# Kernel tuning notes

Measured on AMD Instinct MI355X. Metric: run time of the kernel, lower is better.

Reference implementation:

```python
import jax, jax.numpy as jnp
import numpy as np

D_MODEL, D_STATE, D_CONV, EXPAND = 1024, 16, 4, 2
D_INNER = EXPAND * D_MODEL
DT_RANK = max(16, D_MODEL // 16)
B_SZ, T_LEN = 2, 2048


def setup_inputs() -> dict:
    key = jax.random.key(0)
    ks = jax.random.split(key, 12)
    s = lambda fan: 1.0 / np.sqrt(fan)
    x = jax.random.normal(ks[0], (B_SZ, T_LEN, D_MODEL), jnp.float32)
    sigma2 = jax.random.uniform(ks[1], (B_SZ, T_LEN, 1), jnp.float32)
    W_in = jax.random.normal(ks[2], (D_MODEL, 2 * D_INNER), jnp.float32) * s(D_MODEL)
    conv_w = jax.random.normal(ks[3], (D_CONV, 1, D_INNER), jnp.float32) * s(D_CONV)
    conv_b = jax.random.normal(ks[4], (D_INNER,), jnp.float32) * 0.01
    W_xproj = jax.random.normal(ks[5], (D_INNER, 2 * D_STATE + DT_RANK), jnp.float32) * s(D_INNER)
    W_delta = jax.random.normal(ks[6], (D_MODEL, D_INNER), jnp.float32) * s(D_MODEL)
    b_delta = jax.random.normal(ks[7], (D_INNER,), jnp.float32) * 0.01
    A_log = jnp.log(jnp.tile(jnp.arange(1, D_STATE + 1, dtype=jnp.float32), (D_INNER, 1)))
    D_param = jnp.ones((D_INNER,), jnp.float32)
    W_out = jax.random.normal(ks[8], (D_INNER, D_MODEL), jnp.float32) * s(D_INNER)
    alpha = jnp.float32(1.0)
    return {"x": x, "sigma2": sigma2, "W_in": W_in, "conv_w": conv_w, "conv_b": conv_b,
            "W_xproj": W_xproj, "W_delta": W_delta, "b_delta": b_delta, "A_log": A_log,
            "D_param": D_param, "W_out": W_out, "alpha": alpha}


def _forward(x, sigma2, W_in, conv_w, conv_b, W_xproj, W_delta, b_delta, A_log, D_param, W_out, alpha):
    # in_proj and split
    xz = jnp.einsum('btd,de->bte', x, W_in)
    u, z = jnp.split(xz, 2, axis=-1)                      # (B,T,d_inner) each
    # causal depthwise conv1d (left pad d_conv-1, truncate to T)
    u = jax.lax.conv_general_dilated(
        u, conv_w, window_strides=(1,), padding=[(D_CONV - 1, 0)],
        dimension_numbers=('NHC', 'HIO', 'NHC'), feature_group_count=D_INNER) + conv_b
    u = jax.nn.silu(u)
    # x_proj -> B, C (delta_raw_proj branch is unused in custom-delta path)
    x_dbl = jnp.einsum('bti,ij->btj', u, W_xproj)
    Bp = x_dbl[..., :D_STATE]                              # (B,T,d_state)
    Cp = x_dbl[..., D_STATE:2 * D_STATE]                   # (B,T,d_state)
    # quality-gated custom delta
    delta_raw = jax.nn.softplus(jnp.einsum('btd,di->bti', x, W_delta) + b_delta)
    delta = delta_raw * jnp.exp(-alpha * sigma2)           # (B,T,d_inner)
    A = -jnp.exp(A_log)                                    # (d_inner,d_state)
    # discretize
    dA = jnp.exp(delta[..., None] * A)                     # (B,T,d_inner,d_state)
    dBu = delta[..., None] * Bp[:, :, None, :] * u[..., None]

    def step(h, inp):
        dA_t, dBu_t, c_t = inp                             # (B,di,ds),(B,di,ds),(B,ds)
        h = dA_t * h + dBu_t
        y_t = jnp.sum(h * c_t[:, None, :], axis=-1)        # (B,d_inner)
        return h, y_t

    h0 = jnp.zeros((x.shape[0], D_INNER, D_STATE), dtype=u.dtype)
    _, ys = jax.lax.scan(step, h0, (jnp.moveaxis(dA, 1, 0), jnp.moveaxis(dBu, 1, 0), jnp.moveaxis(Cp, 1, 0)))
    y = jnp.moveaxis(ys, 0, 1) + u * D_param               # (B,T,d_inner)
    y = y * jax.nn.silu(z)
    return jnp.einsum('bti,id->btd', y, W_out)


def reference(x, sigma2, W_in, conv_w, conv_b, W_xproj, W_delta, b_delta, A_log, D_param, W_out, alpha):
    return _forward(x, sigma2, W_in, conv_w, conv_b, W_xproj, W_delta, b_delta, A_log, D_param, W_out, alpha)
```

## Files before the change

### kernel.cpp

```cpp
#include <hip/hip_runtime.h>
#include <math.h>


constexpr int D_MODEL = 1024;
constexpr int D_STATE = 16;
constexpr int D_CONV  = 4;
constexpr int D_INNER = 2048;
constexpr int XPROJ_W = 96;
constexpr int B_SZ = 2, T_LEN = 2048;
constexpr int ROWS = B_SZ * T_LEN;
constexpr int NCHUNK = 64, CHUNK = T_LEN / NCHUNK;

typedef unsigned short ushort_t;
typedef __bf16 bf16x8 __attribute__((ext_vector_type(8)));
typedef float f32x4 __attribute__((ext_vector_type(4)));

__device__ __forceinline__ ushort_t f2bf(float f) {
  unsigned int u = __float_as_uint(f);
  u = (u + 0x7fffu + ((u >> 16) & 1u)) >> 16;
  return (ushort_t)u;
}
__device__ __forceinline__ float bf2f(ushort_t h) {
  return __uint_as_float(((unsigned int)h) << 16);
}

__device__ __forceinline__ void gload16(const void* g, void* l) {
  __builtin_amdgcn_global_load_lds(
      (const __attribute__((address_space(1))) void*)g,
      (__attribute__((address_space(3))) void*)l, 16, 0, 0);
}

__global__ __launch_bounds__(256)
void convert_all_kernel(const float* __restrict__ x,
                        const float* __restrict__ W_in,
                        const float* __restrict__ W_delta,
                        const float* __restrict__ W_out,
                        ushort_t* __restrict__ xb, ushort_t* __restrict__ WiT,
                        ushort_t* __restrict__ WdT, ushort_t* __restrict__ WoT)
{
  __shared__ float tile[32][33];
  const int blk = blockIdx.x;
  const int tid = threadIdx.x;
  if (blk < 4096) {
    const int i = blk * 256 + tid;
    const float4 v = ((const float4*)x)[i];
    ushort_t tmp[4] = {f2bf(v.x), f2bf(v.y), f2bf(v.z), f2bf(v.w)};
    ((uint2*)xb)[i] = *(const uint2*)tmp;
    return;
  }
  const float* in;
  ushort_t* out;
  int R, C, t;
  if (blk < 8192)      { in = W_in;    out = WiT; R = 1024; C = 4096; t = blk - 4096;  }
  else if (blk < 10240){ in = W_delta; out = WdT; R = 1024; C = 2048; t = blk - 8192;  }
  else                 { in = W_out;   out = WoT; R = 2048; C = 1024; t = blk - 10240; }
  const int tpr = C / 32;
  const int c0 = (t % tpr) * 32, r0 = (t / tpr) * 32;
  const int tx = tid & 31, ty = tid >> 5;
#pragma unroll
  for (int i = 0; i < 32; i += 8)
    tile[ty + i][tx] = in[(size_t)(r0 + ty + i) * C + c0 + tx];
  __syncthreads();
#pragma unroll
  for (int i = 0; i < 32; i += 8)
    out[(size_t)(c0 + ty + i) * R + r0 + tx] = f2bf(tile[tx][ty + i]);
}

template <int MODE, int BM>
__global__ __launch_bounds__(256)
void gemm_t(const ushort_t* __restrict__ A, const ushort_t* __restrict__ Bt,
            const int lda, const int ldb, const int KT,
            ushort_t* __restrict__ outB, float* __restrict__ outF,
            const float* __restrict__ bias, const float* __restrict__ sigma2,
            const float* __restrict__ alphap)
{
  constexpr int MREP = (BM == 32) ? 2 : 4;
  constexpr int NREP = (BM == 128) ? 4 : 2;
  constexpr int RT = BM + 128;
  constexpr int CH = RT / 32;

  __shared__ __align__(16) ushort_t As[BM * 64];
  __shared__ __align__(16) ushort_t Bs[128 * 64];
  const int tid = threadIdx.x;
  const int wave = tid >> 6, lane = tid & 63;
  const int lc = lane & 15, lr = lane >> 4;
  const int m0 = blockIdx.y * BM, n0 = blockIdx.x * 128;
  const int N = gridDim.x * 128;
  const int arow = (BM == 128) ? ((wave >> 1) * 64) : 0;
  const int bcol = (BM == 128) ? ((wave & 1) * 64) : (wave * 32);

  f32x4 acc[MREP][NREP];
#pragma unroll
  for (int i = 0; i < MREP; ++i)
#pragma unroll
    for (int j = 0; j < NREP; ++j) acc[i][j] = (f32x4)0.f;

  const int rlane = lane >> 3;
  const int clane = (lane & 7) * 8;

  for (int kt = 0; kt < KT; ++kt) {
    if (kt) __syncthreads();
    const int k0 = kt * 64;
#pragma unroll
    for (int i = 0; i < CH; ++i) {
      const int r0c = (wave * CH + i) * 8;
      if (r0c < BM) {
        gload16(A + (size_t)(m0 + r0c + rlane) * lda + k0 + clane,
                &As[r0c * 64]);
      } else {
        const int br = r0c - BM;
        gload16(Bt + (size_t)(n0 + br + rlane) * ldb + k0 + clane,
                &Bs[br * 64]);
      }
    }
    __syncthreads();
#pragma unroll
    for (int ks = 0; ks < 2; ++ks) {
      bf16x8 af[MREP], bfr[NREP];
#pragma unroll
      for (int mi = 0; mi < MREP; ++mi)
        af[mi] = *(const bf16x8*)
            &As[(arow + mi * 16 + lc) * 64 + ks * 32 + lr * 8];
#pragma unroll
      for (int ni = 0; ni < NREP; ++ni)
        bfr[ni] = *(const bf16x8*)
            &Bs[(bcol + ni * 16 + lc) * 64 + ks * 32 + lr * 8];
#pragma unroll
      for (int mi = 0; mi < MREP; ++mi)
#pragma unroll
        for (int ni = 0; ni < NREP; ++ni)
          acc[mi][ni] = __builtin_amdgcn_mfma_f32_16x16x32_bf16(
              af[mi], bfr[ni], acc[mi][ni], 0, 0, 0);
    }
  }

  const float alphaV = (MODE == 2) ? alphap[0] : 0.f;
#pragma unroll
  for (int mi = 0; mi < MREP; ++mi) {
    const int rowb = m0 + arow + mi * 16 + lr * 4;
#pragma unroll
    for (int ni = 0; ni < NREP; ++ni) {
      const int col = n0 + bcol + ni * 16 + lc;
      f32x4 v = acc[mi][ni];
      if (MODE == 0) {
#pragma unroll
        for (int r = 0; r < 4; ++r)
          outB[(size_t)(rowb + r) * N + col] = f2bf(v[r]);
      } else if (MODE == 2) {
        const float bv = bias[col];
#pragma unroll
        for (int r = 0; r < 4; ++r) {
          const float xv = v[r] + bv;
          const float sp = (xv > 20.f) ? xv : log1pf(__expf(xv));
          outB[(size_t)(rowb + r) * N + col] =
              f2bf(sp * __expf(-alphaV * sigma2[rowb + r]));
        }
      } else {
#pragma unroll
        for (int r = 0; r < 4; ++r)
          outF[(size_t)(rowb + r) * N + col] = v[r];
      }
    }
  }
}

__device__ __forceinline__ void decay_powers(float d, float (&dA)[16])
{
  const float q1 = __expf(-d);
  const float q2 = q1 * q1, q3 = q2 * q1, q4 = q2 * q2;
  const float q8 = q4 * q4, q12 = q8 * q4;
  dA[0] = q1;        dA[1] = q2;        dA[2] = q3;        dA[3] = q4;
  dA[4] = q4 * q1;   dA[5] = q4 * q2;   dA[6] = q4 * q3;   dA[7] = q8;
  dA[8] = q8 * q1;   dA[9] = q8 * q2;   dA[10] = q8 * q3;  dA[11] = q12;
  dA[12] = q12 * q1; dA[13] = q12 * q2; dA[14] = q12 * q3; dA[15] = q12 * q4;
}

__global__ __launch_bounds__(256)
void conv_xproj_kernel(const ushort_t* __restrict__ xzb,
                       const float* __restrict__ cw,
                       const float* __restrict__ cb,
                       const float* __restrict__ Wx,
                       ushort_t* __restrict__ u, float* __restrict__ BC)
{
  __shared__ float us[8][D_INNER];
  __shared__ float red[8][8][32];
  const int tid = threadIdx.x;
  const int b = blockIdx.y;
  const int t0 = blockIdx.x * 8;
  const int ch0 = tid * 8;

  float wtk[4][8], bs[8];
#pragma unroll
  for (int k = 0; k < 4; ++k) {
    float4 wa = *(const float4*)&cw[k * D_INNER + ch0];
    float4 wb = *(const float4*)&cw[k * D_INNER + ch0 + 4];
    wtk[k][0] = wa.x; wtk[k][1] = wa.y; wtk[k][2] = wa.z; wtk[k][3] = wa.w;
    wtk[k][4] = wb.x; wtk[k][5] = wb.y; wtk[k][6] = wb.z; wtk[k][7] = wb.w;
  }
  {
    float4 ba = *(const float4*)&cb[ch0];
    float4 bb = *(const float4*)&cb[ch0 + 4];
    bs[0] = ba.x; bs[1] = ba.y; bs[2] = ba.z; bs[3] = ba.w;
    bs[4] = bb.x; bs[5] = bb.y; bs[6] = bb.z; bs[7] = bb.w;
  }

#pragma unroll
  for (int r = 0; r < 8; ++r) {
    const int t = t0 + r;
    float acc[8];
#pragma unroll
    for (int j = 0; j < 8; ++j) acc[j] = bs[j];
#pragma unroll
    for (int k = 0; k < 4; ++k) {
      const int tt = t + k - 3;
      if (tt >= 0) {
        uint4 raw = *(const uint4*)
            &xzb[(size_t)(b * T_LEN + tt) * (2 * D_INNER) + ch0];
        const ushort_t* hp = (const ushort_t*)&raw;
#pragma unroll
        for (int j = 0; j < 8; ++j)
          acc[j] = fmaf(bf2f(hp[j]), wtk[k][j], acc[j]);
      }
    }
    ushort_t ub[8];
#pragma unroll
    for (int j = 0; j < 8; ++j) {
      const float ss = acc[j] / (1.f + __expf(-acc[j]));
      us[r][ch0 + j] = ss;
      ub[j] = f2bf(ss);
    }
    *(uint4*)&u[(size_t)(b * T_LEN + t) * D_INNER + ch0] = *(const uint4*)ub;
  }
  __syncthreads();

  const int j = tid & 31, chunk = tid >> 5;
  float p[8] = {0.f, 0.f, 0.f, 0.f, 0.f, 0.f, 0.f, 0.f};
  const float* WxC = Wx + j;
  for (int i = 0; i < 256; ++i) {
    const int k = chunk * 256 + i;
    const float w = WxC[(size_t)k * XPROJ_W];
#pragma unroll
    for (int r = 0; r < 8; ++r) p[r] = fmaf(us[r][k], w, p[r]);
  }
#pragma unroll
  for (int r = 0; r < 8; ++r) red[r][chunk][j] = p[r];
  __syncthreads();
  {
    const int r = tid >> 5, jj = tid & 31;
    float ssum = 0.f;
#pragma unroll
    for (int c = 0; c < 8; ++c) ssum += red[r][c][jj];
    BC[(size_t)(b * T_LEN + t0 + r) * 32 + jj] = ssum;
  }
}

__global__ __launch_bounds__(256)
void scan1_kernel(const ushort_t* __restrict__ delta,
                  const ushort_t* __restrict__ u,
                  const float* __restrict__ BC,
                  float* __restrict__ hEnd, float* __restrict__ sumD)
{
  const int c = blockIdx.x * 256 + threadIdx.x;
  const int b = blockIdx.y;
  const int j = blockIdx.z;
  float h[D_STATE];
#pragma unroll
  for (int n = 0; n < D_STATE; ++n) h[n] = 0.f;
  float sd = 0.f;
  const int t0 = j * CHUNK;
  for (int t = t0; t < t0 + CHUNK; ++t) {
    const int row = b * T_LEN + t;
    const float d = bf2f(delta[(size_t)row * D_INNER + c]);
    const float uu = bf2f(u[(size_t)row * D_INNER + c]);
    sd += d;
    const float du = d * uu;
    float dA[16];
    decay_powers(d, dA);
    const float4* bp4 = (const float4*)&BC[(size_t)row * 32];
    float4 b0 = bp4[0], b1 = bp4[1], b2 = bp4[2], b3 = bp4[3];
    const float bp[16] = {b0.x, b0.y, b0.z, b0.w, b1.x, b1.y, b1.z, b1.w,
                          b2.x, b2.y, b2.z, b2.w, b3.x, b3.y, b3.z, b3.w};
#pragma unroll
    for (int n = 0; n < D_STATE; ++n)
      h[n] = fmaf(dA[n], h[n], du * bp[n]);
  }
  const size_t base = ((size_t)b * D_INNER + c) * NCHUNK + j;
#pragma unroll
  for (int n = 0; n < D_STATE; ++n) hEnd[base * 16 + n] = h[n];
  sumD[base] = sd;
}

__global__ __launch_bounds__(256)
void scan2_kernel(float* __restrict__ hEnd, const float* __restrict__ sumD)
{
  const int idx = blockIdx.x * 256 + threadIdx.x;
  const int n = idx & 15;
  const int c = (idx >> 4) & (D_INNER - 1);
  const int b = idx >> 15;
  const float an = -(float)(n + 1);
  float H = 0.f;
  for (int j = 0; j < NCHUNK; ++j) {
    const size_t base = ((size_t)b * D_INNER + c) * NCHUNK + j;
    const float he = hEnd[base * 16 + n];
    const float sd = sumD[base];
    hEnd[base * 16 + n] = H;
    H = fmaf(__expf(an * sd), H, he);
  }
}

__global__ __launch_bounds__(256)
void scan3_kernel(const ushort_t* __restrict__ delta,
                  const ushort_t* __restrict__ u,
                  const float* __restrict__ BC,
                  const float* __restrict__ hStart,
                  const ushort_t* __restrict__ xzb,
                  const float* __restrict__ Dp, ushort_t* __restrict__ yb)
{
  const int c = blockIdx.x * 256 + threadIdx.x;
  const int b = blockIdx.y;
  const int j = blockIdx.z;
  float h[D_STATE];
  const size_t base = ((size_t)b * D_INNER + c) * NCHUNK + j;
#pragma unroll
  for (int n = 0; n < D_STATE; ++n) h[n] = hStart[base * 16 + n];
  const float dpc = Dp[c];
  const int t0 = j * CHUNK;
  for (int t = t0; t < t0 + CHUNK; ++t) {
    const int row = b * T_LEN + t;
    const float d = bf2f(delta[(size_t)row * D_INNER + c]);
    const float uu = bf2f(u[(size_t)row * D_INNER + c]);
    const float du = d * uu;
    float dA[16];
    decay_powers(d, dA);
    const float4* bc4 = (const float4*)&BC[(size_t)row * 32];
    float4 b0 = bc4[0], b1 = bc4[1], b2 = bc4[2], b3 = bc4[3];
    float4 c0 = bc4[4], c1 = bc4[5], c2 = bc4[6], c3 = bc4[7];
    const float bp[16] = {b0.x, b0.y, b0.z, b0.w, b1.x, b1.y, b1.z, b1.w,
                          b2.x, b2.y, b2.z, b2.w, b3.x, b3.y, b3.z, b3.w};
    const float cp[16] = {c0.x, c0.y, c0.z, c0.w, c1.x, c1.y, c1.z, c1.w,
                          c2.x, c2.y, c2.z, c2.w, c3.x, c3.y, c3.z, c3.w};
    float y = 0.f;
#pragma unroll
    for (int n = 0; n < D_STATE; ++n) {
      h[n] = fmaf(dA[n], h[n], du * bp[n]);
      y = fmaf(h[n], cp[n], y);
    }
    y = fmaf(uu, dpc, y);
    const float z = bf2f(xzb[(size_t)row * (2 * D_INNER) + D_INNER + c]);
    y *= z / (1.f + __expf(-z));
    yb[(size_t)row * D_INNER + c] = f2bf(y);
  }
}

extern "C" void kernel_launch(void* const* d_in, const int* in_sizes, int n_in,
                              void* d_out, int out_size, void* d_ws,
                              size_t ws_size, hipStream_t stream)
{
  const float* x       = (const float*)d_in[0];
  const float* sigma2  = (const float*)d_in[1];
  const float* W_in    = (const float*)d_in[2];
  const float* conv_w  = (const float*)d_in[3];
  const float* conv_b  = (const float*)d_in[4];
  const float* W_xproj = (const float*)d_in[5];
  const float* W_delta = (const float*)d_in[6];
  const float* b_delta = (const float*)d_in[7];
  const float* D_param = (const float*)d_in[9];
  const float* W_out   = (const float*)d_in[10];
  const float* alpha   = (const float*)d_in[11];
  float* out = (float*)d_out;

  char* ws = (char*)d_ws;
  ushort_t* xzb  = (ushort_t*)(ws);
  ushort_t* u    = (ushort_t*)(ws + ((size_t)32  << 20));
  ushort_t* dyb  = (ushort_t*)(ws + ((size_t)48  << 20));
  float*    BC   = (float*)   (ws + ((size_t)64  << 20));
  float*    hEnd = (float*)   (ws + ((size_t)65  << 20));
  float*    sumD = (float*)   (ws + ((size_t)81  << 20));
  ushort_t* xb   = (ushort_t*)(ws + ((size_t)82  << 20));
  ushort_t* WiT  = (ushort_t*)(ws + ((size_t)90  << 20));
  ushort_t* WdT  = (ushort_t*)(ws + ((size_t)98  << 20));
  ushort_t* WoT  = (ushort_t*)(ws + ((size_t)102 << 20));
  ushort_t* yb   = (ushort_t*)(ws + ((size_t)106 << 20));

  convert_all_kernel<<<12288, 256, 0, stream>>>(x, W_in, W_delta, W_out, xb,
                                                WiT, WdT, WoT);
  gemm_t<0, 128><<<dim3(4096 / 128, ROWS / 128), 256, 0, stream>>>(
      xb, WiT, 1024, 1024, 16, xzb, nullptr, nullptr, nullptr, nullptr);
  gemm_t<2, 64><<<dim3(2048 / 128, ROWS / 64), 256, 0, stream>>>(
      xb, WdT, 1024, 1024, 16, dyb, nullptr, b_delta, sigma2, alpha);
  conv_xproj_kernel<<<dim3(T_LEN / 8, B_SZ), 256, 0, stream>>>(
      xzb, conv_w, conv_b, W_xproj, u, BC);
  scan1_kernel<<<dim3(D_INNER / 256, B_SZ, NCHUNK), 256, 0, stream>>>(
      dyb, u, BC, hEnd, sumD);
  scan2_kernel<<<(B_SZ * D_INNER * D_STATE) / 256, 256, 0, stream>>>(hEnd,
                                                                     sumD);
  scan3_kernel<<<dim3(D_INNER / 256, B_SZ, NCHUNK), 256, 0, stream>>>(
      dyb, u, BC, hEnd, xzb, D_param, yb);
  gemm_t<1, 32><<<dim3(1024 / 128, ROWS / 32), 256, 0, stream>>>(
      yb, WoT, 2048, 2048, 32, nullptr, out, nullptr, nullptr, nullptr);
}
```

Before: 243.8 us.

## Pipeline GEMM loads with triple buffering and fuse independent stages into combined launches

The GEMM core now uses a three-stage LDS ring with K-step 32, manual vmcnt waits and raw barriers, so global loads overlap MFMA work. Independent work is packed into shared launches: the W_delta and W_out transposes run beside the in_proj GEMM, and the conv+xproj runs beside the delta GEMM. Other changes: the scan chunk count is halved, the conv tile is stored as bf16 in LDS, and the out-projection uses 64-row tiles. The goal is fewer launches, less idle time and better latency hiding. The cost is heterogeneous blocks within a launch, possible load imbalance, and less parallelism in the scan.

```diff
diff --git a/kernel.cpp b/kernel.cpp
--- a/kernel.cpp
+++ b/kernel.cpp
@@ -9,7 +9,7 @@
 constexpr int XPROJ_W = 96;
 constexpr int B_SZ = 2, T_LEN = 2048;
 constexpr int ROWS = B_SZ * T_LEN;
-constexpr int NCHUNK = 64, CHUNK = T_LEN / NCHUNK;
+constexpr int NCHUNK = 32, CHUNK = T_LEN / NCHUNK;
 
 typedef unsigned short ushort_t;
 typedef __bf16 bf16x8 __attribute__((ext_vector_type(8)));
@@ -30,64 +30,32 @@
       (__attribute__((address_space(3))) void*)l, 16, 0, 0);
 }
 
-__global__ __launch_bounds__(256)
-void convert_all_kernel(const float* __restrict__ x,
-                        const float* __restrict__ W_in,
-                        const float* __restrict__ W_delta,
-                        const float* __restrict__ W_out,
-                        ushort_t* __restrict__ xb, ushort_t* __restrict__ WiT,
-                        ushort_t* __restrict__ WdT, ushort_t* __restrict__ WoT)
-{
-  __shared__ float tile[32][33];
-  const int blk = blockIdx.x;
-  const int tid = threadIdx.x;
-  if (blk < 4096) {
-    const int i = blk * 256 + tid;
-    const float4 v = ((const float4*)x)[i];
-    ushort_t tmp[4] = {f2bf(v.x), f2bf(v.y), f2bf(v.z), f2bf(v.w)};
-    ((uint2*)xb)[i] = *(const uint2*)tmp;
-    return;
-  }
-  const float* in;
-  ushort_t* out;
-  int R, C, t;
-  if (blk < 8192)      { in = W_in;    out = WiT; R = 1024; C = 4096; t = blk - 4096;  }
-  else if (blk < 10240){ in = W_delta; out = WdT; R = 1024; C = 2048; t = blk - 8192;  }
-  else                 { in = W_out;   out = WoT; R = 2048; C = 1024; t = blk - 10240; }
-  const int tpr = C / 32;
-  const int c0 = (t % tpr) * 32, r0 = (t / tpr) * 32;
-  const int tx = tid & 31, ty = tid >> 5;
-#pragma unroll
-  for (int i = 0; i < 32; i += 8)
-    tile[ty + i][tx] = in[(size_t)(r0 + ty + i) * C + c0 + tx];
-  __syncthreads();
-#pragma unroll
-  for (int i = 0; i < 32; i += 8)
-    out[(size_t)(c0 + ty + i) * R + r0 + tx] = f2bf(tile[tx][ty + i]);
-}
-
-template <int MODE, int BM>
-__global__ __launch_bounds__(256)
-void gemm_t(const ushort_t* __restrict__ A, const ushort_t* __restrict__ Bt,
-            const int lda, const int ldb, const int KT,
-            ushort_t* __restrict__ outB, float* __restrict__ outF,
-            const float* __restrict__ bias, const float* __restrict__ sigma2,
-            const float* __restrict__ alphap)
-{
-  constexpr int MREP = (BM == 32) ? 2 : 4;
+__device__ __forceinline__ void pipe_barrier() {
+  __builtin_amdgcn_s_barrier();
+  __builtin_amdgcn_sched_barrier(0);
+  asm volatile("" ::: "memory");
+}
+
+template <int BM, int MODE>
+__device__ __forceinline__ void gemm_core(
+    const ushort_t* __restrict__ A, const ushort_t* __restrict__ Bt,
+    const int lda, const int ldb, const int KT, const int m0, const int n0,
+    const int N, ushort_t* lds, const int tid,
+    ushort_t* __restrict__ outB, float* __restrict__ outF,
+    const float* __restrict__ bias, const float* __restrict__ sigma2,
+    const float alphaV)
+{
+  constexpr int GPW  = (BM + 128) / 64;
+  constexpr int BUFE = (BM + 128) * 32;
+  constexpr int MREP = 4;
   constexpr int NREP = (BM == 128) ? 4 : 2;
-  constexpr int RT = BM + 128;
-  constexpr int CH = RT / 32;
-
-  __shared__ __align__(16) ushort_t As[BM * 64];
-  __shared__ __align__(16) ushort_t Bs[128 * 64];
-  const int tid = threadIdx.x;
+
   const int wave = tid >> 6, lane = tid & 63;
   const int lc = lane & 15, lr = lane >> 4;
-  const int m0 = blockIdx.y * BM, n0 = blockIdx.x * 128;
-  const int N = gridDim.x * 128;
   const int arow = (BM == 128) ? ((wave >> 1) * 64) : 0;
   const int bcol = (BM == 128) ? ((wave & 1) * 64) : (wave * 32);
+  const int rlane = lane >> 2;
+  const int clane = (lane & 3) * 8;
 
   f32x4 acc[MREP][NREP];
 #pragma unroll
@@ -95,46 +63,52 @@
 #pragma unroll
     for (int j = 0; j < NREP; ++j) acc[i][j] = (f32x4)0.f;
 
-  const int rlane = lane >> 3;
-  const int clane = (lane & 7) * 8;
-
-  for (int kt = 0; kt < KT; ++kt) {
-    if (kt) __syncthreads();
-    const int k0 = kt * 64;
-#pragma unroll
-    for (int i = 0; i < CH; ++i) {
-      const int r0c = (wave * CH + i) * 8;
-      if (r0c < BM) {
-        gload16(A + (size_t)(m0 + r0c + rlane) * lda + k0 + clane,
-                &As[r0c * 64]);
-      } else {
-        const int br = r0c - BM;
-        gload16(Bt + (size_t)(n0 + br + rlane) * ldb + k0 + clane,
-                &Bs[br * 64]);
-      }
-    }
-    __syncthreads();
-#pragma unroll
-    for (int ks = 0; ks < 2; ++ks) {
-      bf16x8 af[MREP], bfr[NREP];
-#pragma unroll
-      for (int mi = 0; mi < MREP; ++mi)
-        af[mi] = *(const bf16x8*)
-            &As[(arow + mi * 16 + lc) * 64 + ks * 32 + lr * 8];
+  auto stage = [&](int T) {
+    const int k0 = T * 32;
+    ushort_t* base = lds + (T % 3) * BUFE;
+#pragma unroll
+    for (int i = 0; i < GPW; ++i) {
+      const int row0 = (wave + i * 4) * 16;
+      if (row0 < BM)
+        gload16(A + (size_t)(m0 + row0 + rlane) * lda + k0 + clane,
+                base + row0 * 32);
+      else
+        gload16(Bt + (size_t)(n0 + row0 - BM + rlane) * ldb + k0 + clane,
+                base + row0 * 32);
+    }
+  };
+
+  stage(0);
+  stage(1);
+  asm volatile("s_waitcnt vmcnt(%0)" ::"n"(GPW) : "memory");
+  pipe_barrier();
+
+  for (int T = 0; T < KT; ++T) {
+    if (T + 2 < KT) stage(T + 2);
+    const ushort_t* buf = lds + (T % 3) * BUFE;
+    bf16x8 af[MREP], bfr[NREP];
+#pragma unroll
+    for (int mi = 0; mi < MREP; ++mi)
+      af[mi] = *(const bf16x8*)&buf[(arow + mi * 16 + lc) * 32 + lr * 8];
+#pragma unroll
+    for (int ni = 0; ni < NREP; ++ni)
+      bfr[ni] = *(const bf16x8*)
+          &buf[(BM + bcol + ni * 16 + lc) * 32 + lr * 8];
+#pragma unroll
+    for (int mi = 0; mi < MREP; ++mi)
 #pragma unroll
       for (int ni = 0; ni < NREP; ++ni)
-        bfr[ni] = *(const bf16x8*)
-            &Bs[(bcol + ni * 16 + lc) * 64 + ks * 32 + lr * 8];
-#pragma unroll
-      for (int mi = 0; mi < MREP; ++mi)
-#pragma unroll
-        for (int ni = 0; ni < NREP; ++ni)
-          acc[mi][ni] = __builtin_amdgcn_mfma_f32_16x16x32_bf16(
-              af[mi], bfr[ni], acc[mi][ni], 0, 0, 0);
-    }
-  }
-
-  const float alphaV = (MODE == 2) ? alphap[0] : 0.f;
+        acc[mi][ni] = __builtin_amdgcn_mfma_f32_16x16x32_bf16(
+            af[mi], bfr[ni], acc[mi][ni], 0, 0, 0);
+    if (T + 1 < KT) {
+      if (T + 2 < KT)
+        asm volatile("s_waitcnt vmcnt(%0)" ::"n"(GPW) : "memory");
+      else
+        asm volatile("s_waitcnt vmcnt(0)" ::: "memory");
+      pipe_barrier();
+    }
+  }
+
 #pragma unroll
   for (int mi = 0; mi < MREP; ++mi) {
     const int rowb = m0 + arow + mi * 16 + lr * 4;
@@ -164,6 +138,166 @@
   }
 }
 
+__device__ __forceinline__ void xpose_tile(const float* in, ushort_t* out,
+                                           int R, int C, int t, int tid,
+                                           char* smem)
+{
+  float (*tile)[33] = (float (*)[33])smem;
+  const int tpr = C / 32;
+  const int c0 = (t % tpr) * 32, r0 = (t / tpr) * 32;
+  const int tx = tid & 31, ty = tid >> 5;
+#pragma unroll
+  for (int i = 0; i < 32; i += 8)
+    tile[ty + i][tx] = in[(size_t)(r0 + ty + i) * C + c0 + tx];
+  __syncthreads();
+#pragma unroll
+  for (int i = 0; i < 32; i += 8)
+    out[(size_t)(c0 + ty + i) * R + r0 + tx] = f2bf(tile[tx][ty + i]);
+}
+
+__global__ __launch_bounds__(256)
+void convert_x_wi_kernel(const float* __restrict__ x,
+                         const float* __restrict__ W_in,
+                         ushort_t* __restrict__ xb, ushort_t* __restrict__ WiT)
+{
+  __shared__ __align__(16) char smem[4224];
+  const int blk = blockIdx.x, tid = threadIdx.x;
+  if (blk < 4096) {
+    const int i = blk * 256 + tid;
+    const float4 v = ((const float4*)x)[i];
+    ushort_t tmp[4] = {f2bf(v.x), f2bf(v.y), f2bf(v.z), f2bf(v.w)};
+    ((uint2*)xb)[i] = *(const uint2*)tmp;
+    return;
+  }
+  xpose_tile(W_in, WiT, 1024, 4096, blk - 4096, tid, smem);
+}
+
+__global__ __launch_bounds__(256)
+void gemm1_xpose_kernel(const ushort_t* __restrict__ A,
+                        const ushort_t* __restrict__ Bt,
+                        ushort_t* __restrict__ outB,
+                        const float* __restrict__ W_delta,
+                        const float* __restrict__ W_out,
+                        ushort_t* __restrict__ WdT, ushort_t* __restrict__ WoT)
+{
+  __shared__ __align__(16) char smem[49152];
+  const int bid = blockIdx.x, tid = threadIdx.x;
+  if (bid >= 1024) {
+    int t = bid - 1024;
+    if (t < 2048) xpose_tile(W_delta, WdT, 1024, 2048, t, tid, smem);
+    else          xpose_tile(W_out,   WoT, 2048, 1024, t - 2048, tid, smem);
+    return;
+  }
+  gemm_core<128, 0>(A, Bt, 1024, 1024, 32, (bid >> 5) * 128,
+                    (bid & 31) * 128, 4096, (ushort_t*)smem, tid, outB,
+                    nullptr, nullptr, nullptr, 0.f);
+}
+
+__global__ __launch_bounds__(256)
+void conv_gemm2_kernel(const ushort_t* __restrict__ xzb,
+                       const float* __restrict__ cw,
+                       const float* __restrict__ cb,
+                       const float* __restrict__ Wx,
+                       ushort_t* __restrict__ u, float* __restrict__ BC,
+                       const ushort_t* __restrict__ A,
+                       const ushort_t* __restrict__ WdT,
+                       ushort_t* __restrict__ dyb,
+                       const float* __restrict__ bias,
+                       const float* __restrict__ sigma2,
+                       const float* __restrict__ alphap)
+{
+  __shared__ __align__(16) char smem[40960];
+  const int bid = blockIdx.x, tid = threadIdx.x;
+
+  if (bid < 512) {
+    ushort_t (*usb)[D_INNER] = (ushort_t (*)[D_INNER])smem;
+    float (*red)[8][32] = (float (*)[8][32])(smem + 32768);
+    const int b = bid & 1;
+    const int t0 = (bid >> 1) * 8;
+    const int ch0 = tid * 8;
+
+    float wtk[4][8], bsv[8];
+#pragma unroll
+    for (int k = 0; k < 4; ++k) {
+      float4 wa = *(const float4*)&cw[k * D_INNER + ch0];
+      float4 wb = *(const float4*)&cw[k * D_INNER + ch0 + 4];
+      wtk[k][0] = wa.x; wtk[k][1] = wa.y; wtk[k][2] = wa.z; wtk[k][3] = wa.w;
+      wtk[k][4] = wb.x; wtk[k][5] = wb.y; wtk[k][6] = wb.z; wtk[k][7] = wb.w;
+    }
+    {
+      float4 ba = *(const float4*)&cb[ch0];
+      float4 bb = *(const float4*)&cb[ch0 + 4];
+      bsv[0] = ba.x; bsv[1] = ba.y; bsv[2] = ba.z; bsv[3] = ba.w;
+      bsv[4] = bb.x; bsv[5] = bb.y; bsv[6] = bb.z; bsv[7] = bb.w;
+    }
+#pragma unroll
+    for (int r = 0; r < 8; ++r) {
+      const int t = t0 + r;
+      float acc[8];
+#pragma unroll
+      for (int j = 0; j < 8; ++j) acc[j] = bsv[j];
+#pragma unroll
+      for (int k = 0; k < 4; ++k) {
+        const int tt = t + k - 3;
+        if (tt >= 0) {
+          uint4 raw = *(const uint4*)
+              &xzb[(size_t)(b * T_LEN + tt) * (2 * D_INNER) + ch0];
+          const ushort_t* hp = (const ushort_t*)&raw;
+#pragma unroll
+          for (int j = 0; j < 8; ++j)
+            acc[j] = fmaf(bf2f(hp[j]), wtk[k][j], acc[j]);
+        }
+      }
+      ushort_t ub[8];
+#pragma unroll
+      for (int j = 0; j < 8; ++j) {
+        const float ss = acc[j] / (1.f + __expf(-acc[j]));
+        ub[j] = f2bf(ss);
+      }
+      *(uint4*)&usb[r][ch0] = *(const uint4*)ub;
+      *(uint4*)&u[(size_t)(b * T_LEN + t) * D_INNER + ch0] = *(const uint4*)ub;
+    }
+    __syncthreads();
+
+    const int j = tid & 31, chunk = tid >> 5;
+    float p[8] = {0.f, 0.f, 0.f, 0.f, 0.f, 0.f, 0.f, 0.f};
+    const float* WxC = Wx + j;
+    for (int i = 0; i < 256; ++i) {
+      const int k = chunk * 256 + i;
+      const float w = WxC[(size_t)k * XPROJ_W];
+#pragma unroll
+      for (int r = 0; r < 8; ++r)
+        p[r] = fmaf(bf2f(usb[r][k]), w, p[r]);
+    }
+#pragma unroll
+    for (int r = 0; r < 8; ++r) red[r][chunk][j] = p[r];
+    __syncthreads();
+    {
+      const int r = tid >> 5, jj = tid & 31;
+      float ssum = 0.f;
+#pragma unroll
+      for (int c = 0; c < 8; ++c) ssum += red[r][c][jj];
+      BC[(size_t)(b * T_LEN + t0 + r) * 32 + jj] = ssum;
+    }
+    return;
+  }
+
+  const int gidx = bid - 512;
+  gemm_core<64, 2>(A, WdT, 1024, 1024, 32, (gidx >> 4) * 64,
+                   (gidx & 15) * 128, 2048, (ushort_t*)smem, tid, dyb,
+                   nullptr, bias, sigma2, alphap[0]);
+}
+
+__global__ __launch_bounds__(256)
+void gemm3_kernel(const ushort_t* __restrict__ A,
+                  const ushort_t* __restrict__ Bt, float* __restrict__ out)
+{
+  __shared__ __align__(16) char smem[36864];
+  gemm_core<64, 1>(A, Bt, 2048, 2048, 64, (int)blockIdx.y * 64,
+                   (int)blockIdx.x * 128, 1024, (ushort_t*)smem,
+                   (int)threadIdx.x, nullptr, out, nullptr, nullptr, 0.f);
+}
+
 __device__ __forceinline__ void decay_powers(float d, float (&dA)[16])
 {
   const float q1 = __expf(-d);
@@ -173,85 +307,6 @@
   dA[4] = q4 * q1;   dA[5] = q4 * q2;   dA[6] = q4 * q3;   dA[7] = q8;
   dA[8] = q8 * q1;   dA[9] = q8 * q2;   dA[10] = q8 * q3;  dA[11] = q12;
   dA[12] = q12 * q1; dA[13] = q12 * q2; dA[14] = q12 * q3; dA[15] = q12 * q4;
-}
-
-__global__ __launch_bounds__(256)
-void conv_xproj_kernel(const ushort_t* __restrict__ xzb,
-                       const float* __restrict__ cw,
-                       const float* __restrict__ cb,
-                       const float* __restrict__ Wx,
-                       ushort_t* __restrict__ u, float* __restrict__ BC)
-{
-  __shared__ float us[8][D_INNER];
-  __shared__ float red[8][8][32];
-  const int tid = threadIdx.x;
-  const int b = blockIdx.y;
-  const int t0 = blockIdx.x * 8;
-  const int ch0 = tid * 8;
-
-  float wtk[4][8], bs[8];
-#pragma unroll
-  for (int k = 0; k < 4; ++k) {
-    float4 wa = *(const float4*)&cw[k * D_INNER + ch0];
-    float4 wb = *(const float4*)&cw[k * D_INNER + ch0 + 4];
-    wtk[k][0] = wa.x; wtk[k][1] = wa.y; wtk[k][2] = wa.z; wtk[k][3] = wa.w;
-    wtk[k][4] = wb.x; wtk[k][5] = wb.y; wtk[k][6] = wb.z; wtk[k][7] = wb.w;
-  }
-  {
-    float4 ba = *(const float4*)&cb[ch0];
-    float4 bb = *(const float4*)&cb[ch0 + 4];
-    bs[0] = ba.x; bs[1] = ba.y; bs[2] = ba.z; bs[3] = ba.w;
-    bs[4] = bb.x; bs[5] = bb.y; bs[6] = bb.z; bs[7] = bb.w;
-  }
-
-#pragma unroll
-  for (int r = 0; r < 8; ++r) {
-    const int t = t0 + r;
-    float acc[8];
-#pragma unroll
-    for (int j = 0; j < 8; ++j) acc[j] = bs[j];
-#pragma unroll
-    for (int k = 0; k < 4; ++k) {
-      const int tt = t + k - 3;
-      if (tt >= 0) {
-        uint4 raw = *(const uint4*)
-            &xzb[(size_t)(b * T_LEN + tt) * (2 * D_INNER) + ch0];
-        const ushort_t* hp = (const ushort_t*)&raw;
-#pragma unroll
-        for (int j = 0; j < 8; ++j)
-          acc[j] = fmaf(bf2f(hp[j]), wtk[k][j], acc[j]);
-      }
-    }
-    ushort_t ub[8];
-#pragma unroll
-    for (int j = 0; j < 8; ++j) {
-      const float ss = acc[j] / (1.f + __expf(-acc[j]));
-      us[r][ch0 + j] = ss;
-      ub[j] = f2bf(ss);
-    }
-    *(uint4*)&u[(size_t)(b * T_LEN + t) * D_INNER + ch0] = *(const uint4*)ub;
-  }
-  __syncthreads();
-
-  const int j = tid & 31, chunk = tid >> 5;
-  float p[8] = {0.f, 0.f, 0.f, 0.f, 0.f, 0.f, 0.f, 0.f};
-  const float* WxC = Wx + j;
-  for (int i = 0; i < 256; ++i) {
-    const int k = chunk * 256 + i;
-    const float w = WxC[(size_t)k * XPROJ_W];
-#pragma unroll
-    for (int r = 0; r < 8; ++r) p[r] = fmaf(us[r][k], w, p[r]);
-  }
-#pragma unroll
-  for (int r = 0; r < 8; ++r) red[r][chunk][j] = p[r];
-  __syncthreads();
-  {
-    const int r = tid >> 5, jj = tid & 31;
-    float ssum = 0.f;
-#pragma unroll
-    for (int c = 0; c < 8; ++c) ssum += red[r][c][jj];
-    BC[(size_t)(b * T_LEN + t0 + r) * 32 + jj] = ssum;
-  }
 }
 
 __global__ __launch_bounds__(256)
@@ -375,27 +430,24 @@
   ushort_t* dyb  = (ushort_t*)(ws + ((size_t)48  << 20));
   float*    BC   = (float*)   (ws + ((size_t)64  << 20));
   float*    hEnd = (float*)   (ws + ((size_t)65  << 20));
-  float*    sumD = (float*)   (ws + ((size_t)81  << 20));
-  ushort_t* xb   = (ushort_t*)(ws + ((size_t)82  << 20));
-  ushort_t* WiT  = (ushort_t*)(ws + ((size_t)90  << 20));
-  ushort_t* WdT  = (ushort_t*)(ws + ((size_t)98  << 20));
-  ushort_t* WoT  = (ushort_t*)(ws + ((size_t)102 << 20));
-  ushort_t* yb   = (ushort_t*)(ws + ((size_t)106 << 20));
-
-  convert_all_kernel<<<12288, 256, 0, stream>>>(x, W_in, W_delta, W_out, xb,
-                                                WiT, WdT, WoT);
-  gemm_t<0, 128><<<dim3(4096 / 128, ROWS / 128), 256, 0, stream>>>(
-      xb, WiT, 1024, 1024, 16, xzb, nullptr, nullptr, nullptr, nullptr);
-  gemm_t<2, 64><<<dim3(2048 / 128, ROWS / 64), 256, 0, stream>>>(
-      xb, WdT, 1024, 1024, 16, dyb, nullptr, b_delta, sigma2, alpha);
-  conv_xproj_kernel<<<dim3(T_LEN / 8, B_SZ), 256, 0, stream>>>(
-      xzb, conv_w, conv_b, W_xproj, u, BC);
+  float*    sumD = (float*)   (ws + ((size_t)82  << 20));
+  ushort_t* xb   = (ushort_t*)(ws + ((size_t)84  << 20));
+  ushort_t* WiT  = (ushort_t*)(ws + ((size_t)92  << 20));
+  ushort_t* WdT  = (ushort_t*)(ws + ((size_t)100 << 20));
+  ushort_t* WoT  = (ushort_t*)(ws + ((size_t)104 << 20));
+  ushort_t* yb   = (ushort_t*)(ws + ((size_t)108 << 20));
+
+  convert_x_wi_kernel<<<8192, 256, 0, stream>>>(x, W_in, xb, WiT);
+  gemm1_xpose_kernel<<<5120, 256, 0, stream>>>(xb, WiT, xzb, W_delta, W_out,
+                                               WdT, WoT);
+  conv_gemm2_kernel<<<1536, 256, 0, stream>>>(xzb, conv_w, conv_b, W_xproj, u,
+                                              BC, xb, WdT, dyb, b_delta,
+                                              sigma2, alpha);
   scan1_kernel<<<dim3(D_INNER / 256, B_SZ, NCHUNK), 256, 0, stream>>>(
       dyb, u, BC, hEnd, sumD);
   scan2_kernel<<<(B_SZ * D_INNER * D_STATE) / 256, 256, 0, stream>>>(hEnd,
                                                                      sumD);
   scan3_kernel<<<dim3(D_INNER / 256, B_SZ, NCHUNK), 256, 0, stream>>>(
       dyb, u, BC, hEnd, xzb, D_param, yb);
-  gemm_t<1, 32><<<dim3(1024 / 128, ROWS / 32), 256, 0, stream>>>(
-      yb, WoT, 2048, 2048, 32, nullptr, out, nullptr, nullptr, nullptr);
-}
+  gemm3_kernel<<<dim3(1024 / 128, ROWS / 64), 256, 0, stream>>>(yb, WoT, out);
+}
```

Result: faster. 216.7 us, median of 2 (-11.1%).
